# Kernel optimization log

Hardware: AMD Instinct MI355X
Metric: run time of the kernel (lower is better)

## Reference

```python
import jax, jax.numpy as jnp
import numpy as np

B, C, H, W = 4, 256, 64, 64
GROUPS = 32
EPS = 1e-5


def setup_inputs() -> dict:
    key = jax.random.key(0)
    ks = jax.random.split(key, 8)
    s = 1.0 / np.sqrt(C)
    return {
        "Hand": jax.random.normal(ks[0], (B, C, H, W), jnp.float32),
        "U": jax.random.normal(ks[1], (B, C, H, W), jnp.float32),
        "WH_w": jax.random.normal(ks[2], (C, C), jnp.float32) * s,
        "WH_b": jax.random.normal(ks[3], (C,), jnp.float32) * 0.01,
        "WU_w": jax.random.normal(ks[4], (C, C), jnp.float32) * s,
        "WU_b": jax.random.normal(ks[5], (C,), jnp.float32) * 0.01,
        "gn_w": jax.random.normal(ks[6], (C,), jnp.float32) * 0.1,
        "gn_b": jax.random.normal(ks[7], (C,), jnp.float32) * 0.1,
    }


def _group_norm(x, w, b):
    # x: [B, C, H, W], normalize within each of GROUPS channel groups over (C//G, H, W)
    b_, c_, h_, w_ = x.shape
    xg = x.reshape(b_, GROUPS, c_ // GROUPS, h_, w_)
    mean = jnp.mean(xg, axis=(2, 3, 4), keepdims=True)
    var = jnp.var(xg, axis=(2, 3, 4), keepdims=True)
    xn = ((xg - mean) * jax.lax.rsqrt(var + EPS)).reshape(b_, c_, h_, w_)
    return xn * w[None, :, None, None] + b[None, :, None, None]


def reference(Hand, U, WH_w, WH_b, WU_w, WU_b, gn_w, gn_b):
    b_, c_, h_, w_ = Hand.shape
    n = h_ * w_
    Hf = Hand.reshape(b_, c_, n)  # [B, C, N]
    Uf = U.reshape(b_, c_, n)     # [B, C, N]
    # 1x1 convs == per-pixel linear on channels
    q = jnp.einsum('oc,bcn->bon', WH_w, Hf) + WH_b[None, :, None]  # [B, C, N]
    k = jnp.einsum('oc,bcn->bon', WU_w, Uf) + WU_b[None, :, None]  # [B, C, N]
    # affinity: A[b, n, m] = sum_c q[b,c,n] * k[b,c,m]  (unscaled)
    A = jnp.einsum('bcn,bcm->bnm', q, k)  # [B, N, N]
    A = jax.nn.softmax(A, axis=-1)
    out = jnp.einsum('bnm,bcm->bcn', A, Uf).reshape(b_, c_, h_, w_)
    return _group_norm(out, gn_w, gn_b) + Hand
```

## Files before the change

kernel.cpp:

```cpp
#include <hip/hip_runtime.h>
#include <hip/hip_fp16.h>
#include <math.h>


typedef _Float16 v8h __attribute__((ext_vector_type(8)));
typedef float    v4f __attribute__((ext_vector_type(4)));

#define NB 4
#define NC 256
#define NS 4096
#define NG 32
#define GEPS 1e-5f
#define NSPLIT 3
#define KSTRIDE 272
#define KTILE   8704
#define PSTRIDE 40

#define ASYNC_BARRIER() asm volatile("s_waitcnt lgkmcnt(0)\n\ts_barrier" ::: "memory")

template <int CTRL>
__device__ __forceinline__ float dpp_rot(float x) {
    int r = __builtin_amdgcn_update_dpp(__float_as_int(x), __float_as_int(x),
                                        CTRL, 0xF, 0xF, false);
    return __int_as_float(r);
}
__device__ __forceinline__ float row_max16(float x) {
    x = fmaxf(x, dpp_rot<0x128>(x));
    x = fmaxf(x, dpp_rot<0x124>(x));
    x = fmaxf(x, dpp_rot<0x122>(x));
    x = fmaxf(x, dpp_rot<0x121>(x));
    return x;
}
__device__ __forceinline__ float row_sum16(float x) {
    x = x + dpp_rot<0x128>(x);
    x = x + dpp_rot<0x124>(x);
    x = x + dpp_rot<0x122>(x);
    x = x + dpp_rot<0x121>(x);
    return x;
}

__global__ __launch_bounds__(256) void k_convert(const float* __restrict__ Wh,
    const float* __restrict__ Wu, _Float16* __restrict__ Wh16, _Float16* __restrict__ Wu16)
{
    const int i = blockIdx.x * 256 + threadIdx.x;
    const int o = i >> 8, c = i & 255;
    const int idx = ((((o >> 4) * 8 + (c >> 5)) * 4 + ((c >> 3) & 3)) * 16
                     + (o & 15)) * 8 + (c & 7);
    Wh16[idx] = (_Float16)Wh[i];
    Wu16[idx] = (_Float16)Wu[i];
}

__global__ __launch_bounds__(256) void k_qkgemm(const float* __restrict__ Hand,
    const float* __restrict__ U, const _Float16* __restrict__ Wh16,
    const _Float16* __restrict__ Wu16, const float* __restrict__ WHb,
    const float* __restrict__ WUb, _Float16* __restrict__ qT,
    _Float16* __restrict__ kTsw, _Float16* __restrict__ Uh)
{
    const int nt = blockIdx.x, b = blockIdx.y, z = blockIdx.z;
    const float*    X    = z ? U    : Hand;
    const _Float16* W    = z ? Wu16 : Wh16;
    const float*    bias = z ? WUb  : WHb;

    const int tid = threadIdx.x, w = tid >> 6, lane = tid & 63;
    const int q4 = lane >> 4, l15 = lane & 15;
    const int n = nt * 64 + w * 16 + l15;

    const float* Xcol = X + (size_t)b * NC * NS + n;
    v8h A[8];
#pragma unroll
    for (int kc = 0; kc < 8; ++kc) {
        const int c0 = kc * 32 + q4 * 8;
        v8h a;
#pragma unroll
        for (int j = 0; j < 8; ++j) a[j] = (_Float16)Xcol[(size_t)(c0 + j) * NS];
        A[kc] = a;
    }

    if (z == 1) {
        _Float16* ub = Uh + (size_t)b * NC * NS + n;
#pragma unroll
        for (int kc = 0; kc < 8; ++kc) {
            const int c0 = kc * 32 + q4 * 8;
#pragma unroll
            for (int j = 0; j < 8; ++j) ub[(size_t)(c0 + j) * NS] = A[kc][j];
        }
    }

#pragma unroll 4
    for (int osub = 0; osub < 16; ++osub) {
        const int o = osub * 16 + l15;
        v4f acc = {0.f, 0.f, 0.f, 0.f};
#pragma unroll
        for (int kc = 0; kc < 8; ++kc) {
            const v8h bf = *(const v8h*)(W + ((size_t)(osub * 8 + kc) * 64 + lane) * 8);
            acc = __builtin_amdgcn_mfma_f32_16x16x32_f16(A[kc], bf, acc, 0, 0, 0);
        }
        const float bv = bias[o];
        if (z == 0) {
            _Float16* orow = qT + ((size_t)b * NS + nt * 64 + w * 16 + q4 * 4) * NC + o;
#pragma unroll
            for (int r = 0; r < 4; ++r) orow[(size_t)r * NC] = (_Float16)(acc[r] + bv);
        } else {
            _Float16* kb = kTsw + (size_t)b * 128 * KTILE;
#pragma unroll
            for (int r = 0; r < 4; ++r) {
                const int m = nt * 64 + w * 16 + q4 * 4 + r;
                kb[(size_t)(m >> 5) * KTILE + (m & 31) * KSTRIDE + o] = (_Float16)(acc[r] + bv);
            }
        }
    }
}

__global__ __launch_bounds__(256, 3) void k_attn(const _Float16* __restrict__ qT,
    const _Float16* __restrict__ kTsw, const _Float16* __restrict__ Uh,
    _Float16* __restrict__ Ppart, float* __restrict__ mstat, float* __restrict__ lstat)
{
    const int b  = blockIdx.x;
    const int nt = blockIdx.y;
    const int s  = blockIdx.z;
    const int t0 = (s == 0) ? 0 : (s == 1 ? 43 : 86);
    const int t1 = (s == 2) ? 128 : t0 + 43;

    __shared__ __align__(16) _Float16 Klds[2][KTILE];
    __shared__ __align__(16) _Float16 Plds[64 * PSTRIDE];
    __shared__ __align__(16) float alphaS[64];

    const int tid = threadIdx.x, w = tid >> 6, lane = tid & 63;
    const int q4 = lane >> 4, l15 = lane & 15;

    const _Float16* kTb = kTsw + (size_t)b * 128 * KTILE;
    const _Float16* Uhb = Uh + (size_t)b * NC * NS;

    {
        const _Float16* src = kTb + (size_t)t0 * KTILE;
#pragma unroll
        for (int j = 0; j < 5; ++j) {
            const int ch = (w * 5 + j) % 17;
            __builtin_amdgcn_global_load_lds(
                (const __attribute__((address_space(1))) void*)(src + ch * 512 + lane * 8),
                (__attribute__((address_space(3))) void*)(&Klds[t0 & 1][ch * 512]), 16, 0, 0);
        }
    }

    v8h Q[8];
    {
        const _Float16* qrow = qT + ((size_t)b * NS + nt * 64 + w * 16 + l15) * NC;
#pragma unroll
        for (int kc = 0; kc < 8; ++kc) Q[kc] = *(const v8h*)(qrow + kc * 32 + q4 * 8);
    }

    v4f O[4][4];
#pragma unroll
    for (int i = 0; i < 4; ++i)
#pragma unroll
        for (int j = 0; j < 4; ++j) O[i][j] = (v4f){0.f, 0.f, 0.f, 0.f};
    float mi[4] = {-INFINITY, -INFINITY, -INFINITY, -INFINITY};
    float li[4] = {0.f, 0.f, 0.f, 0.f};

    for (int t = t0; t < t1; ++t) {
        const int p = t & 1;
        const int m0 = t * 32;

        v8h Ur[4];
#pragma unroll
        for (int js = 0; js < 4; ++js)
            Ur[js] = *(const v8h*)(Uhb + (size_t)(w * 64 + js * 16 + l15) * NS + m0 + q4 * 8);
        asm volatile("" ::: "memory");

        {
            const int tn = (t + 1 < t1) ? t + 1 : t0;
            const _Float16* src = kTb + (size_t)tn * KTILE;
#pragma unroll
            for (int j = 0; j < 5; ++j) {
                const int ch = (w * 5 + j) % 17;
                __builtin_amdgcn_global_load_lds(
                    (const __attribute__((address_space(1))) void*)(src + ch * 512 + lane * 8),
                    (__attribute__((address_space(3))) void*)(&Klds[p ^ 1][ch * 512]), 16, 0, 0);
            }
        }

        asm volatile("s_waitcnt vmcnt(9)" ::: "memory");
        ASYNC_BARRIER();

        v4f sv[2];
        sv[0] = (v4f){0.f, 0.f, 0.f, 0.f};
        sv[1] = (v4f){0.f, 0.f, 0.f, 0.f};
#pragma unroll
        for (int kc = 0; kc < 8; ++kc) {
#pragma unroll
            for (int ms = 0; ms < 2; ++ms) {
                const v8h kf = *(const v8h*)(&Klds[p][(ms * 16 + l15) * KSTRIDE
                                             + (kc * 4 + q4) * 8]);
                sv[ms] = __builtin_amdgcn_mfma_f32_16x16x32_f16(Q[kc], kf, sv[ms], 0, 0, 0);
            }
        }

        float al[4];
#pragma unroll
        for (int r = 0; r < 4; ++r) {
            const float tm = row_max16(fmaxf(sv[0][r], sv[1][r]));
            const float mn = fmaxf(mi[r], tm);
            al[r] = __expf(mi[r] - mn);
            mi[r] = mn;
            const float p0 = __expf(sv[0][r] - mn);
            const float p1 = __expf(sv[1][r] - mn);
            sv[0][r] = p0; sv[1][r] = p1;
            li[r] = li[r] * al[r] + p0 + p1;
        }
        if (l15 == 0) {
#pragma unroll
            for (int r = 0; r < 4; ++r) alphaS[w * 16 + q4 * 4 + r] = al[r];
        }
#pragma unroll
        for (int ms = 0; ms < 2; ++ms)
#pragma unroll
            for (int r = 0; r < 4; ++r) {
                const int row = w * 16 + q4 * 4 + r;
                Plds[row * PSTRIDE + ms * 16 + l15] = (_Float16)sv[ms][r];
            }
        ASYNC_BARRIER();

#pragma unroll
        for (int is = 0; is < 4; ++is) {
            const float4 av = *(const float4*)&alphaS[is * 16 + q4 * 4];
            const v4f aa = {av.x, av.y, av.z, av.w};
#pragma unroll
            for (int js = 0; js < 4; ++js) O[is][js] *= aa;
        }
#pragma unroll
        for (int is = 0; is < 4; ++is) {
            const v8h Pf = *(const v8h*)(&Plds[(is * 16 + l15) * PSTRIDE + q4 * 8]);
#pragma unroll
            for (int js = 0; js < 4; ++js)
                O[is][js] = __builtin_amdgcn_mfma_f32_16x16x32_f16(Pf, Ur[js], O[is][js], 0, 0, 0);
        }
    }

    asm volatile("s_waitcnt vmcnt(0)" ::: "memory");

#pragma unroll
    for (int r = 0; r < 4; ++r) li[r] = row_sum16(li[r]);
    if (l15 == 0) {
#pragma unroll
        for (int r = 0; r < 4; ++r) {
            const int n = nt * 64 + w * 16 + q4 * 4 + r;
            mstat[(size_t)(s * NB + b) * NS + n] = mi[r];
            lstat[(size_t)(s * NB + b) * NS + n] = li[r];
        }
    }
#pragma unroll
    for (int is = 0; is < 4; ++is)
#pragma unroll
        for (int js = 0; js < 4; ++js)
#pragma unroll
            for (int r = 0; r < 4; ++r) {
                _Float16* dst = Ppart + ((size_t)(s * NB + b) * NS + nt * 64 + is * 16
                                         + q4 * 4 + r) * NC + w * 64 + js * 16 + l15;
                __builtin_nontemporal_store((_Float16)O[is][js][r], dst);
            }
}

__global__ __launch_bounds__(256) void k_merge(const _Float16* __restrict__ Pp,
    const float* __restrict__ mstat, const float* __restrict__ lstat,
    float* __restrict__ Opre, float* __restrict__ statacc)
{
    const int b = blockIdx.y, tid = threadIdx.x;
    const int n = blockIdx.x * 8 + (tid >> 5);
    const int c0 = (tid & 31) * 8;
    const size_t nb = (size_t)b * NS + n;
    const size_t SP = (size_t)NB * NS;
    const float m0 = mstat[nb], m1 = mstat[SP + nb], m2 = mstat[2 * SP + nb];
    const float l0 = lstat[nb], l1 = lstat[SP + nb], l2 = lstat[2 * SP + nb];
    const float M  = fmaxf(m0, fmaxf(m1, m2));
    const float e0 = __expf(m0 - M), e1 = __expf(m1 - M), e2 = __expf(m2 - M);
    const float inv = 1.f / (e0 * l0 + e1 * l1 + e2 * l2);
    const float w0 = e0 * inv, w1 = e1 * inv, w2 = e2 * inv;
    const size_t base = nb * NC + c0;
    const v8h p0 = *(const v8h*)(Pp + base);
    const v8h p1 = *(const v8h*)(Pp + SP * NC + base);
    const v8h p2 = *(const v8h*)(Pp + 2 * SP * NC + base);
    float v[8];
    float s1 = 0.f, s2 = 0.f;
#pragma unroll
    for (int j = 0; j < 8; ++j) {
        v[j] = w0 * (float)p0[j] + w1 * (float)p1[j] + w2 * (float)p2[j];
        s1 += v[j]; s2 += v[j] * v[j];
    }
    *(float4*)(Opre + base)     = make_float4(v[0], v[1], v[2], v[3]);
    *(float4*)(Opre + base + 4) = make_float4(v[4], v[5], v[6], v[7]);

    __shared__ float r1[256], r2[256];
    r1[tid] = s1; r2[tid] = s2;
    __syncthreads();
    if (tid < 32) {
        float a = 0.f, q = 0.f;
#pragma unroll
        for (int k = 0; k < 8; ++k) { a += r1[tid + 32 * k]; q += r2[tid + 32 * k]; }
        atomicAdd(&statacc[(b * NG + tid) * 2 + 0], a);
        atomicAdd(&statacc[(b * NG + tid) * 2 + 1], q);
    }
}

__global__ __launch_bounds__(256) void k_gnapply(const float* __restrict__ Opre,
    const float* __restrict__ Hand, const float* __restrict__ gnw,
    const float* __restrict__ gnb, const float* __restrict__ statacc,
    float* __restrict__ out)
{
    const int nt = blockIdx.x, ct = blockIdx.y, b = blockIdx.z;
    __shared__ float buf[64 * 65];
    const int tid = threadIdx.x;
    {
        const int nr = tid >> 4, c4 = (tid & 15) * 4;
#pragma unroll
        for (int k = 0; k < 4; ++k) {
            const int n = nr + 16 * k;
            const float4 v = *(const float4*)(Opre + ((size_t)b * NS + nt * 64 + n) * NC
                                              + ct * 64 + c4);
            buf[n * 65 + c4 + 0] = v.x; buf[n * 65 + c4 + 1] = v.y;
            buf[n * 65 + c4 + 2] = v.z; buf[n * 65 + c4 + 3] = v.w;
        }
    }
    __syncthreads();
    const int nw = tid & 63, c0 = tid >> 6;
#pragma unroll
    for (int k = 0; k < 16; ++k) {
        const int cl = c0 + 4 * k;
        const int c  = ct * 64 + cl;
        const int g  = c >> 3;
        const float s1   = statacc[(b * NG + g) * 2 + 0];
        const float s2   = statacc[(b * NG + g) * 2 + 1];
        const float mean = s1 * (1.f / 32768.f);
        const float var  = s2 * (1.f / 32768.f) - mean * mean;
        const float rstd = rsqrtf(var + GEPS);
        const size_t oidx = ((size_t)b * NC + c) * NS + nt * 64 + nw;
        out[oidx] = (buf[nw * 65 + cl] - mean) * rstd * gnw[c] + gnb[c] + Hand[oidx];
    }
}

extern "C" void kernel_launch(void* const* d_in, const int* in_sizes, int n_in,
                              void* d_out, int out_size, void* d_ws, size_t ws_size,
                              hipStream_t stream)
{
    const float* Hand = (const float*)d_in[0];
    const float* U    = (const float*)d_in[1];
    const float* WHw  = (const float*)d_in[2];
    const float* WHb  = (const float*)d_in[3];
    const float* WUw  = (const float*)d_in[4];
    const float* WUb  = (const float*)d_in[5];
    const float* gnw  = (const float*)d_in[6];
    const float* gnb  = (const float*)d_in[7];
    float* out = (float*)d_out;

    char* ws = (char*)d_ws;
    _Float16* qT     = (_Float16*)(ws);
    _Float16* kTsw   = (_Float16*)(ws + 8388608);
    _Float16* Uh     = (_Float16*)(ws + 17301504);
    _Float16* Wh16   = (_Float16*)(ws + 25690112);
    _Float16* Wu16   = (_Float16*)(ws + 25821184);
    float*    mstat  = (float*)(ws + 25952256);
    float*    lstat  = (float*)(ws + 26148864);
    float*    statacc= (float*)(ws + 26345472);
    _Float16* Ppart  = (_Float16*)(ws + 26347520);
    float*    Opre   = (float*)(ws);

    hipMemsetAsync(statacc, 0, NB * NG * 2 * sizeof(float), stream);
    k_convert<<<dim3((NC * NC) / 256), 256, 0, stream>>>(WHw, WUw, Wh16, Wu16);
    k_qkgemm <<<dim3(64, NB, 2), 256, 0, stream>>>(Hand, U, Wh16, Wu16, WHb, WUb, qT, kTsw, Uh);
    k_attn   <<<dim3(NB, 64, NSPLIT), 256, 0, stream>>>(qT, kTsw, Uh, Ppart, mstat, lstat);
    k_merge  <<<dim3(NS / 8, NB), 256, 0, stream>>>(Ppart, mstat, lstat, Opre, statacc);
    k_gnapply<<<dim3(64, 4, NB), 256, 0, stream>>>(Opre, Hand, gnw, gnb, statacc, out);
}
```

Measured before the change: 272.6 us.

## Use exp2 softmax with lazy max rescaling and double-buffered P tiles

Folds log2(e) into q at projection time so the attention softmax uses exp2 directly. Adds lazy max updates: the running max is only raised when a row's tile max exceeds it by a threshold, and the O rescale is skipped when all alphas are one. P and alpha shared buffers are double-buffered so one barrier per iteration is removed, and the U loads are moved after the K prefetch with adjusted vmcnt waits. Partial outputs are normalized by l before the fp16 store, and the merge weights change to match. The threshold lets unnormalized exponentials grow up to 2^11 before rescaling, which risks fp16 range and precision in P.

```diff
diff --git a/kernel.cpp b/kernel.cpp
--- a/kernel.cpp
+++ b/kernel.cpp
@@ -15,6 +15,8 @@
 #define KSTRIDE 272
 #define KTILE   8704
 #define PSTRIDE 40
+#define THR2    11.0f
+#define LOG2E   1.44269504f
 
 #define ASYNC_BARRIER() asm volatile("s_waitcnt lgkmcnt(0)\n\ts_barrier" ::: "memory")
 
@@ -99,7 +101,8 @@
         if (z == 0) {
             _Float16* orow = qT + ((size_t)b * NS + nt * 64 + w * 16 + q4 * 4) * NC + o;
 #pragma unroll
-            for (int r = 0; r < 4; ++r) orow[(size_t)r * NC] = (_Float16)(acc[r] + bv);
+            for (int r = 0; r < 4; ++r)
+                orow[(size_t)r * NC] = (_Float16)((acc[r] + bv) * LOG2E);
         } else {
             _Float16* kb = kTsw + (size_t)b * 128 * KTILE;
 #pragma unroll
@@ -122,8 +125,9 @@
     const int t1 = (s == 2) ? 128 : t0 + 43;
 
     __shared__ __align__(16) _Float16 Klds[2][KTILE];
-    __shared__ __align__(16) _Float16 Plds[64 * PSTRIDE];
-    __shared__ __align__(16) float alphaS[64];
+    __shared__ __align__(16) _Float16 Plds[2][64 * PSTRIDE];
+    __shared__ __align__(16) float alphaS[2][64];
+    __shared__ __align__(16) float liS[64];
 
     const int tid = threadIdx.x, w = tid >> 6, lane = tid & 63;
     const int q4 = lane >> 4, l15 = lane & 15;
@@ -141,6 +145,7 @@
                 (__attribute__((address_space(3))) void*)(&Klds[t0 & 1][ch * 512]), 16, 0, 0);
         }
     }
+    asm volatile("" ::: "memory");
 
     v8h Q[8];
     {
@@ -148,6 +153,10 @@
 #pragma unroll
         for (int kc = 0; kc < 8; ++kc) Q[kc] = *(const v8h*)(qrow + kc * 32 + q4 * 8);
     }
+    asm volatile("" ::: "memory");
+
+    asm volatile("s_waitcnt vmcnt(8)" ::: "memory");
+    ASYNC_BARRIER();
 
     v4f O[4][4];
 #pragma unroll
@@ -160,12 +169,6 @@
     for (int t = t0; t < t1; ++t) {
         const int p = t & 1;
         const int m0 = t * 32;
-
-        v8h Ur[4];
-#pragma unroll
-        for (int js = 0; js < 4; ++js)
-            Ur[js] = *(const v8h*)(Uhb + (size_t)(w * 64 + js * 16 + l15) * NS + m0 + q4 * 8);
-        asm volatile("" ::: "memory");
 
         {
             const int tn = (t + 1 < t1) ? t + 1 : t0;
@@ -178,9 +181,13 @@
                     (__attribute__((address_space(3))) void*)(&Klds[p ^ 1][ch * 512]), 16, 0, 0);
             }
         }
-
-        asm volatile("s_waitcnt vmcnt(9)" ::: "memory");
-        ASYNC_BARRIER();
+        asm volatile("" ::: "memory");
+
+        v8h Ur[4];
+#pragma unroll
+        for (int js = 0; js < 4; ++js)
+            Ur[js] = *(const v8h*)(Uhb + (size_t)(w * 64 + js * 16 + l15) * NS + m0 + q4 * 8);
+        asm volatile("" ::: "memory");
 
         v4f sv[2];
         sv[0] = (v4f){0.f, 0.f, 0.f, 0.f};
@@ -195,41 +202,67 @@
             }
         }
 
+        float tm[4];
+        int upd = 0;
+#pragma unroll
+        for (int r = 0; r < 4; ++r) {
+            tm[r] = row_max16(fmaxf(sv[0][r], sv[1][r]));
+            upd |= (tm[r] > mi[r] + THR2) ? 1 : 0;
+        }
         float al[4];
+        if (__any(upd)) {
+#pragma unroll
+            for (int r = 0; r < 4; ++r) {
+                const float mn = fmaxf(mi[r], tm[r]);
+                al[r] = __builtin_amdgcn_exp2f(mi[r] - mn);
+                mi[r] = mn;
+            }
+        } else {
+#pragma unroll
+            for (int r = 0; r < 4; ++r) al[r] = 1.f;
+        }
+        if (l15 == 0) {
+#pragma unroll
+            for (int r = 0; r < 4; ++r) alphaS[p][w * 16 + q4 * 4 + r] = al[r];
+        }
 #pragma unroll
         for (int r = 0; r < 4; ++r) {
-            const float tm = row_max16(fmaxf(sv[0][r], sv[1][r]));
-            const float mn = fmaxf(mi[r], tm);
-            al[r] = __expf(mi[r] - mn);
-            mi[r] = mn;
-            const float p0 = __expf(sv[0][r] - mn);
-            const float p1 = __expf(sv[1][r] - mn);
+            const float p0 = __builtin_amdgcn_exp2f(sv[0][r] - mi[r]);
+            const float p1 = __builtin_amdgcn_exp2f(sv[1][r] - mi[r]);
             sv[0][r] = p0; sv[1][r] = p1;
-            li[r] = li[r] * al[r] + p0 + p1;
-        }
-        if (l15 == 0) {
-#pragma unroll
-            for (int r = 0; r < 4; ++r) alphaS[w * 16 + q4 * 4 + r] = al[r];
+            li[r] = li[r] * al[r] + (p0 + p1);
         }
 #pragma unroll
         for (int ms = 0; ms < 2; ++ms)
 #pragma unroll
             for (int r = 0; r < 4; ++r) {
                 const int row = w * 16 + q4 * 4 + r;
-                Plds[row * PSTRIDE + ms * 16 + l15] = (_Float16)sv[ms][r];
-            }
+                Plds[p][row * PSTRIDE + ms * 16 + l15] = (_Float16)sv[ms][r];
+            }
+
+        asm volatile("s_waitcnt vmcnt(4)" ::: "memory");
         ASYNC_BARRIER();
 
+        float4 av[4];
+#pragma unroll
+        for (int is = 0; is < 4; ++is)
+            av[is] = *(const float4*)&alphaS[p][is * 16 + q4 * 4];
+        int ne = 0;
+#pragma unroll
+        for (int is = 0; is < 4; ++is)
+            ne |= (av[is].x != 1.f || av[is].y != 1.f ||
+                   av[is].z != 1.f || av[is].w != 1.f) ? 1 : 0;
+        if (__any(ne)) {
+#pragma unroll
+            for (int is = 0; is < 4; ++is) {
+                const v4f aa = {av[is].x, av[is].y, av[is].z, av[is].w};
+#pragma unroll
+                for (int js = 0; js < 4; ++js) O[is][js] *= aa;
+            }
+        }
 #pragma unroll
         for (int is = 0; is < 4; ++is) {
-            const float4 av = *(const float4*)&alphaS[is * 16 + q4 * 4];
-            const v4f aa = {av.x, av.y, av.z, av.w};
-#pragma unroll
-            for (int js = 0; js < 4; ++js) O[is][js] *= aa;
-        }
-#pragma unroll
-        for (int is = 0; is < 4; ++is) {
-            const v8h Pf = *(const v8h*)(&Plds[(is * 16 + l15) * PSTRIDE + q4 * 8]);
+            const v8h Pf = *(const v8h*)(&Plds[p][(is * 16 + l15) * PSTRIDE + q4 * 8]);
 #pragma unroll
             for (int js = 0; js < 4; ++js)
                 O[is][js] = __builtin_amdgcn_mfma_f32_16x16x32_f16(Pf, Ur[js], O[is][js], 0, 0, 0);
@@ -246,18 +279,25 @@
             const int n = nt * 64 + w * 16 + q4 * 4 + r;
             mstat[(size_t)(s * NB + b) * NS + n] = mi[r];
             lstat[(size_t)(s * NB + b) * NS + n] = li[r];
-        }
-    }
-#pragma unroll
-    for (int is = 0; is < 4; ++is)
-#pragma unroll
-        for (int js = 0; js < 4; ++js)
+            liS[w * 16 + q4 * 4 + r] = li[r];
+        }
+    }
+    ASYNC_BARRIER();
+#pragma unroll
+    for (int is = 0; is < 4; ++is) {
+        const float4 lv = *(const float4*)&liS[is * 16 + q4 * 4];
+        const v4f invv = {1.f / lv.x, 1.f / lv.y, 1.f / lv.z, 1.f / lv.w};
+#pragma unroll
+        for (int js = 0; js < 4; ++js) {
+            const v4f ov = O[is][js] * invv;
 #pragma unroll
             for (int r = 0; r < 4; ++r) {
                 _Float16* dst = Ppart + ((size_t)(s * NB + b) * NS + nt * 64 + is * 16
                                          + q4 * 4 + r) * NC + w * 64 + js * 16 + l15;
-                __builtin_nontemporal_store((_Float16)O[is][js][r], dst);
-            }
+                __builtin_nontemporal_store((_Float16)ov[r], dst);
+            }
+        }
+    }
 }
 
 __global__ __launch_bounds__(256) void k_merge(const _Float16* __restrict__ Pp,
@@ -272,9 +312,9 @@
     const float m0 = mstat[nb], m1 = mstat[SP + nb], m2 = mstat[2 * SP + nb];
     const float l0 = lstat[nb], l1 = lstat[SP + nb], l2 = lstat[2 * SP + nb];
     const float M  = fmaxf(m0, fmaxf(m1, m2));
-    const float e0 = __expf(m0 - M), e1 = __expf(m1 - M), e2 = __expf(m2 - M);
+    const float e0 = exp2f(m0 - M), e1 = exp2f(m1 - M), e2 = exp2f(m2 - M);
     const float inv = 1.f / (e0 * l0 + e1 * l1 + e2 * l2);
-    const float w0 = e0 * inv, w1 = e1 * inv, w2 = e2 * inv;
+    const float w0 = e0 * l0 * inv, w1 = e1 * l1 * inv, w2 = e2 * l2 * inv;
     const size_t base = nb * NC + c0;
     const v8h p0 = *(const v8h*)(Pp + base);
     const v8h p1 = *(const v8h*)(Pp + SP * NC + base);
```

Measured after the change: 305.3 us. +12.0%, slower.

## Use four-way KV split, exp2 softmax with prescaled Q, and MFMA priority hints

Applied to the files above, without the earlier changes.

Raises the attention key-split count from 3 to 4 when the workspace is large enough, so the grid has 1024 blocks instead of 768, and sets launch bounds to 4 blocks per CU. Q is prescaled by log2(e) in the projection so the softmax can use the native exp2 instruction. MFMA sections are wrapped in s_setprio to favour matrix issue. The merge kernel is templated over the split count, which adds partial-output traffic for the extra split, and the higher occupancy target may cause register pressure or spills.

```diff
diff --git a/kernel.cpp b/kernel.cpp
--- a/kernel.cpp
+++ b/kernel.cpp
@@ -11,10 +11,10 @@
 #define NS 4096
 #define NG 32
 #define GEPS 1e-5f
-#define NSPLIT 3
 #define KSTRIDE 272
 #define KTILE   8704
 #define PSTRIDE 40
+#define LOG2E   1.44269504f
 
 #define ASYNC_BARRIER() asm volatile("s_waitcnt lgkmcnt(0)\n\ts_barrier" ::: "memory")
 
@@ -99,7 +99,8 @@
         if (z == 0) {
             _Float16* orow = qT + ((size_t)b * NS + nt * 64 + w * 16 + q4 * 4) * NC + o;
 #pragma unroll
-            for (int r = 0; r < 4; ++r) orow[(size_t)r * NC] = (_Float16)(acc[r] + bv);
+            for (int r = 0; r < 4; ++r)
+                orow[(size_t)r * NC] = (_Float16)((acc[r] + bv) * LOG2E);
         } else {
             _Float16* kb = kTsw + (size_t)b * 128 * KTILE;
 #pragma unroll
@@ -111,15 +112,16 @@
     }
 }
 
-__global__ __launch_bounds__(256, 3) void k_attn(const _Float16* __restrict__ qT,
+template <int NSPL>
+__global__ __launch_bounds__(256, 4) void k_attn(const _Float16* __restrict__ qT,
     const _Float16* __restrict__ kTsw, const _Float16* __restrict__ Uh,
     _Float16* __restrict__ Ppart, float* __restrict__ mstat, float* __restrict__ lstat)
 {
     const int b  = blockIdx.x;
     const int nt = blockIdx.y;
     const int s  = blockIdx.z;
-    const int t0 = (s == 0) ? 0 : (s == 1 ? 43 : 86);
-    const int t1 = (s == 2) ? 128 : t0 + 43;
+    const int t0 = (s * 128) / NSPL;
+    const int t1 = ((s + 1) * 128) / NSPL;
 
     __shared__ __align__(16) _Float16 Klds[2][KTILE];
     __shared__ __align__(16) _Float16 Plds[64 * PSTRIDE];
@@ -185,6 +187,7 @@
         v4f sv[2];
         sv[0] = (v4f){0.f, 0.f, 0.f, 0.f};
         sv[1] = (v4f){0.f, 0.f, 0.f, 0.f};
+        __builtin_amdgcn_s_setprio(1);
 #pragma unroll
         for (int kc = 0; kc < 8; ++kc) {
 #pragma unroll
@@ -194,16 +197,17 @@
                 sv[ms] = __builtin_amdgcn_mfma_f32_16x16x32_f16(Q[kc], kf, sv[ms], 0, 0, 0);
             }
         }
+        __builtin_amdgcn_s_setprio(0);
 
         float al[4];
 #pragma unroll
         for (int r = 0; r < 4; ++r) {
             const float tm = row_max16(fmaxf(sv[0][r], sv[1][r]));
             const float mn = fmaxf(mi[r], tm);
-            al[r] = __expf(mi[r] - mn);
+            al[r] = __builtin_amdgcn_exp2f(mi[r] - mn);
             mi[r] = mn;
-            const float p0 = __expf(sv[0][r] - mn);
-            const float p1 = __expf(sv[1][r] - mn);
+            const float p0 = __builtin_amdgcn_exp2f(sv[0][r] - mn);
+            const float p1 = __builtin_amdgcn_exp2f(sv[1][r] - mn);
             sv[0][r] = p0; sv[1][r] = p1;
             li[r] = li[r] * al[r] + p0 + p1;
         }
@@ -227,6 +231,7 @@
 #pragma unroll
             for (int js = 0; js < 4; ++js) O[is][js] *= aa;
         }
+        __builtin_amdgcn_s_setprio(1);
 #pragma unroll
         for (int is = 0; is < 4; ++is) {
             const v8h Pf = *(const v8h*)(&Plds[(is * 16 + l15) * PSTRIDE + q4 * 8]);
@@ -234,6 +239,7 @@
             for (int js = 0; js < 4; ++js)
                 O[is][js] = __builtin_amdgcn_mfma_f32_16x16x32_f16(Pf, Ur[js], O[is][js], 0, 0, 0);
         }
+        __builtin_amdgcn_s_setprio(0);
     }
 
     asm volatile("s_waitcnt vmcnt(0)" ::: "memory");
@@ -260,6 +266,7 @@
             }
 }
 
+template <int NSPL>
 __global__ __launch_bounds__(256) void k_merge(const _Float16* __restrict__ Pp,
     const float* __restrict__ mstat, const float* __restrict__ lstat,
     float* __restrict__ Opre, float* __restrict__ statacc)
@@ -269,23 +276,36 @@
     const int c0 = (tid & 31) * 8;
     const size_t nb = (size_t)b * NS + n;
     const size_t SP = (size_t)NB * NS;
-    const float m0 = mstat[nb], m1 = mstat[SP + nb], m2 = mstat[2 * SP + nb];
-    const float l0 = lstat[nb], l1 = lstat[SP + nb], l2 = lstat[2 * SP + nb];
-    const float M  = fmaxf(m0, fmaxf(m1, m2));
-    const float e0 = __expf(m0 - M), e1 = __expf(m1 - M), e2 = __expf(m2 - M);
-    const float inv = 1.f / (e0 * l0 + e1 * l1 + e2 * l2);
-    const float w0 = e0 * inv, w1 = e1 * inv, w2 = e2 * inv;
+
+    float m[NSPL], l[NSPL];
+#pragma unroll
+    for (int sp = 0; sp < NSPL; ++sp) {
+        m[sp] = mstat[sp * SP + nb];
+        l[sp] = lstat[sp * SP + nb];
+    }
+    float M = m[0];
+#pragma unroll
+    for (int sp = 1; sp < NSPL; ++sp) M = fmaxf(M, m[sp]);
+    float denom = 0.f, wgt[NSPL];
+#pragma unroll
+    for (int sp = 0; sp < NSPL; ++sp) {
+        wgt[sp] = exp2f(m[sp] - M);
+        denom += wgt[sp] * l[sp];
+    }
+    const float inv = 1.f / denom;
+
     const size_t base = nb * NC + c0;
-    const v8h p0 = *(const v8h*)(Pp + base);
-    const v8h p1 = *(const v8h*)(Pp + SP * NC + base);
-    const v8h p2 = *(const v8h*)(Pp + 2 * SP * NC + base);
-    float v[8];
+    float v[8] = {0.f, 0.f, 0.f, 0.f, 0.f, 0.f, 0.f, 0.f};
+#pragma unroll
+    for (int sp = 0; sp < NSPL; ++sp) {
+        const float ws = wgt[sp] * inv;
+        const v8h pv = *(const v8h*)(Pp + (size_t)sp * SP * NC + base);
+#pragma unroll
+        for (int j = 0; j < 8; ++j) v[j] += ws * (float)pv[j];
+    }
     float s1 = 0.f, s2 = 0.f;
 #pragma unroll
-    for (int j = 0; j < 8; ++j) {
-        v[j] = w0 * (float)p0[j] + w1 * (float)p1[j] + w2 * (float)p2[j];
-        s1 += v[j]; s2 += v[j] * v[j];
-    }
+    for (int j = 0; j < 8; ++j) { s1 += v[j]; s2 += v[j] * v[j]; }
     *(float4*)(Opre + base)     = make_float4(v[0], v[1], v[2], v[3]);
     *(float4*)(Opre + base + 4) = make_float4(v[4], v[5], v[6], v[7]);
 
@@ -351,22 +371,31 @@
     const float* gnb  = (const float*)d_in[7];
     float* out = (float*)d_out;
 
+    const size_t NEED4 = 25952256u + 2u * 262144u + 2048u + 33554432u;
+    const int nsplit = (ws_size >= NEED4) ? 4 : 3;
+
     char* ws = (char*)d_ws;
     _Float16* qT     = (_Float16*)(ws);
     _Float16* kTsw   = (_Float16*)(ws + 8388608);
     _Float16* Uh     = (_Float16*)(ws + 17301504);
     _Float16* Wh16   = (_Float16*)(ws + 25690112);
     _Float16* Wu16   = (_Float16*)(ws + 25821184);
+    const size_t statB = (size_t)nsplit * NB * NS * 4;
     float*    mstat  = (float*)(ws + 25952256);
-    float*    lstat  = (float*)(ws + 26148864);
-    float*    statacc= (float*)(ws + 26345472);
-    _Float16* Ppart  = (_Float16*)(ws + 26347520);
+    float*    lstat  = (float*)(ws + 25952256 + statB);
+    float*    statacc= (float*)(ws + 25952256 + 2 * statB);
+    _Float16* Ppart  = (_Float16*)(ws + 25952256 + 2 * statB + 2048);
     float*    Opre   = (float*)(ws);
 
     hipMemsetAsync(statacc, 0, NB * NG * 2 * sizeof(float), stream);
     k_convert<<<dim3((NC * NC) / 256), 256, 0, stream>>>(WHw, WUw, Wh16, Wu16);
     k_qkgemm <<<dim3(64, NB, 2), 256, 0, stream>>>(Hand, U, Wh16, Wu16, WHb, WUb, qT, kTsw, Uh);
-    k_attn   <<<dim3(NB, 64, NSPLIT), 256, 0, stream>>>(qT, kTsw, Uh, Ppart, mstat, lstat);
-    k_merge  <<<dim3(NS / 8, NB), 256, 0, stream>>>(Ppart, mstat, lstat, Opre, statacc);
+    if (nsplit == 4) {
+        k_attn<4> <<<dim3(NB, 64, 4), 256, 0, stream>>>(qT, kTsw, Uh, Ppart, mstat, lstat);
+        k_merge<4><<<dim3(NS / 8, NB), 256, 0, stream>>>(Ppart, mstat, lstat, Opre, statacc);
+    } else {
+        k_attn<3> <<<dim3(NB, 64, 3), 256, 0, stream>>>(qT, kTsw, Uh, Ppart, mstat, lstat);
+        k_merge<3><<<dim3(NS / 8, NB), 256, 0, stream>>>(Ppart, mstat, lstat, Opre, statacc);
+    }
     k_gnapply<<<dim3(64, 4, NB), 256, 0, stream>>>(Opre, Hand, gnw, gnb, statacc, out);
 }
```

Measured after the change: 393.7 us. +44.4%, slower.
